# Kernel optimization log

Measured on AMD Instinct MI355X. Metric: run time of the kernel, lower is better.

## Reference

```python
import jax, jax.numpy as jnp
import numpy as np

EMBED = 64
OUT = 64
KERW = 64
DIM = 3

def setup_inputs() -> dict:
    key = jax.random.key(0)
    ks = jax.random.split(key, 6)
    x = jax.random.normal(ks[0], (8, 4096, EMBED), dtype=jnp.float32)
    grid = jax.random.uniform(ks[1], (8, 4096, DIM), dtype=jnp.float32)
    # DenseNet([dim, ker_width_l, output_size*embed_size], GELU): two Linear layers,
    # GELU between, no activation after the last layer.
    W1 = jax.random.normal(ks[2], (DIM, KERW), dtype=jnp.float32) / np.sqrt(DIM)
    b1 = jnp.zeros((KERW,), dtype=jnp.float32)
    W2 = jax.random.normal(ks[3], (KERW, OUT * EMBED), dtype=jnp.float32) / np.sqrt(KERW)
    b2 = jnp.zeros((OUT * EMBED,), dtype=jnp.float32)
    return {"x": x, "grid": grid, "W1": W1, "b1": b1, "W2": W2, "b2": b2}

def reference(x, grid, W1, b1, W2, b2):
    shape = x.shape
    # generator MLP: grid [.., dim] -> per-point weight [.., embed*out]
    h = jax.nn.gelu(grid @ W1 + b1, approximate=False)
    weight = h @ W2 + b2                              # [B, P, embed*out]
    weight = weight.reshape(-1, EMBED, OUT)           # [N, embed, out]
    xf = x.reshape(-1, shape[-1])                     # [N, embed]
    out = jnp.einsum('bi,bio->bo', xf, weight)        # [N, out]
    return out.reshape(*shape[:-1], OUT)
```

## Files before the change

### kernel.cpp

```cpp
#include <hip/hip_runtime.h>
#include <hip/hip_fp16.h>

typedef _Float16 f16x8 __attribute__((ext_vector_type(8)));
typedef float f32x4 __attribute__((ext_vector_type(4)));

#define N_PTS 32768
#define ROWS 64
#define X_STRIDE 72
#define P_STRIDE 68

__global__ __launch_bounds__(256) void prep_kernel(
    const float* __restrict__ W2, const float* __restrict__ b2,
    _Float16* __restrict__ wsB) {
  __shared__ _Float16 w_lds[64][X_STRIDE];
  const int c   = blockIdx.x;
  const int tid = threadIdx.x;
  {
    const float* src = (c < 64) ? (W2 + c * 4096 + tid * 16) : (b2 + tid * 16);
    int kl = tid >> 2, o = (tid & 3) * 16;
    f16x8 v0, v1;
    #pragma unroll
    for (int j = 0; j < 8; ++j) {
      v0[j] = (_Float16)src[j];
      v1[j] = (_Float16)src[8 + j];
    }
    *(f16x8*)(&w_lds[kl][o])     = v0;
    *(f16x8*)(&w_lds[kl][o + 8]) = v1;
  }
  __syncthreads();
  #pragma unroll
  for (int u = 0; u < 2; ++u) {
    int t = tid + u * 256;
    int q = t >> 6, lane = t & 63;
    int klbase = (q >> 2) * 32 + ((lane >> 4) & 3) * 8;
    int o      = (q & 3) * 16 + (lane & 15);
    f16x8 v;
    #pragma unroll
    for (int j = 0; j < 8; ++j) v[j] = w_lds[klbase + j][o];
    *(f16x8*)(wsB + c * 4096 + t * 8) = v;
  }
}

__global__ __launch_bounds__(256) void main_kernel(
    const float* __restrict__ x, const float* __restrict__ gridp,
    const float* __restrict__ W1, const float* __restrict__ b1,
    const _Float16* __restrict__ wsB, float* __restrict__ out) {

  __shared__ _Float16 h_t[4][ROWS][16];
  __shared__ float part[4][ROWS * P_STRIDE];
  _Float16* x_lds = (_Float16*)&part[0][0];

  const int tid  = threadIdx.x;
  const int lane = tid & 63;
  const int wave = tid >> 6;
  const int rowblk = blockIdx.x * ROWS;

  const float* xsrc = x + rowblk * 64 + tid * 16;
  f32x4 xr0 = *(const f32x4*)(xsrc);
  f32x4 xr1 = *(const f32x4*)(xsrc + 4);
  f32x4 xr2 = *(const f32x4*)(xsrc + 8);
  f32x4 xr3 = *(const f32x4*)(xsrc + 12);

  {
    int row = tid >> 2;
    int w4  = tid & 3;
    int r = rowblk + row;
    float g0 = gridp[r * 3 + 0], g1 = gridp[r * 3 + 1], g2 = gridp[r * 3 + 2];
    f16x8 h0, h1;
    #pragma unroll
    for (int q = 0; q < 16; ++q) {
      int k = w4 + 4 * q;
      float v = g0 * W1[k] + g1 * W1[64 + k] + g2 * W1[128 + k] + b1[k];
      float v2 = v * v;
      float u  = v * fmaf(0.044715f, v2, 1.0f);
      float e  = __builtin_amdgcn_exp2f(u * 2.3022084f);
      float rr = e + 1.0f;
      float inv;
      asm("v_rcp_f32 %0, %1" : "=v"(inv) : "v"(rr));
      float h = v * (1.0f - inv);
      if (q < 8) h0[q] = (_Float16)h; else h1[q - 8] = (_Float16)h;
    }
    *(f16x8*)(&h_t[w4][row][0]) = h0;
    *(f16x8*)(&h_t[w4][row][8]) = h1;
  }

  {
    int row = tid >> 2, o = (tid & 3) * 16;
    f16x8 v0, v1;
    #pragma unroll
    for (int j = 0; j < 4; ++j) {
      v0[j]     = (_Float16)xr0[j];
      v0[4 + j] = (_Float16)xr1[j];
      v1[j]     = (_Float16)xr2[j];
      v1[4 + j] = (_Float16)xr3[j];
    }
    *(f16x8*)(&x_lds[row * X_STRIDE + o])     = v0;
    *(f16x8*)(&x_lds[row * X_STRIDE + o + 8]) = v1;
  }
  __syncthreads();

  const int mrow = lane & 15;
  const int kgrp = lane >> 4;
  const _Float16* bp = wsB + lane * 8;

  auto LOADB = [&](f16x8* b, int c) {
    #pragma unroll
    for (int q = 0; q < 8; ++q)
      b[q] = *(const f16x8*)(bp + (c * 8 + q) * 512);
  };

  f16x8 bA[8], bB[8], bC[8];
  LOADB(bA, wave);
  LOADB(bB, wave + 4);
  LOADB(bC, wave + 8);

  f16x8 hreg[4][2];
  #pragma unroll
  for (int m = 0; m < 4; ++m) {
    hreg[m][0] = *(const f16x8*)(&h_t[wave][m * 16 + mrow][0]);
    hreg[m][1] = *(const f16x8*)(&h_t[wave][m * 16 + mrow][8]);
  }

  f16x8 xf[4][2];
  #pragma unroll
  for (int m = 0; m < 4; ++m)
    #pragma unroll
    for (int s = 0; s < 2; ++s)
      xf[m][s] = *(const f16x8*)(&x_lds[(m * 16 + mrow) * X_STRIDE + s * 32 + kgrp * 8]);

  f32x4 acc[4][4];
  #pragma unroll
  for (int m = 0; m < 4; ++m)
    #pragma unroll
    for (int n = 0; n < 4; ++n)
      acc[m][n] = (f32x4){0.f, 0.f, 0.f, 0.f};

  auto COMPUTE = [&](const f16x8* b, int p) {
    __builtin_amdgcn_s_setprio(1);
    #pragma unroll
    for (int m = 0; m < 4; ++m) {
      _Float16 hh = hreg[m][p >> 3][p & 7];
      f16x8 hs = {hh, hh, hh, hh, hh, hh, hh, hh};
      f16x8 a0 = xf[m][0] * hs;
      f16x8 a1 = xf[m][1] * hs;
      #pragma unroll
      for (int n = 0; n < 4; ++n) {
        acc[m][n] = __builtin_amdgcn_mfma_f32_16x16x32_f16(a0, b[n],     acc[m][n], 0, 0, 0);
        acc[m][n] = __builtin_amdgcn_mfma_f32_16x16x32_f16(a1, b[4 + n], acc[m][n], 0, 0, 0);
      }
    }
    __builtin_amdgcn_s_setprio(0);
  };
  auto COMPUTE_BIAS = [&](const f16x8* b) {
    __builtin_amdgcn_s_setprio(1);
    #pragma unroll
    for (int m = 0; m < 4; ++m)
      #pragma unroll
      for (int n = 0; n < 4; ++n) {
        acc[m][n] = __builtin_amdgcn_mfma_f32_16x16x32_f16(xf[m][0], b[n],     acc[m][n], 0, 0, 0);
        acc[m][n] = __builtin_amdgcn_mfma_f32_16x16x32_f16(xf[m][1], b[4 + n], acc[m][n], 0, 0, 0);
      }
    __builtin_amdgcn_s_setprio(0);
  };

  #pragma unroll
  for (int g = 0; g < 5; ++g) {
    COMPUTE(bA, 3 * g);
    if (3 * g + 3 < 16) LOADB(bA, wave + 4 * (3 * g + 3));
    COMPUTE(bB, 3 * g + 1);
    if (3 * g + 4 < 16) LOADB(bB, wave + 4 * (3 * g + 4));
    else if (wave == 0) LOADB(bB, 64);
    COMPUTE(bC, 3 * g + 2);
    if (3 * g + 5 < 16) LOADB(bC, wave + 4 * (3 * g + 5));
  }
  COMPUTE(bA, 15);
  if (wave == 0) COMPUTE_BIAS(bB);

  __syncthreads();

  {
    float* pw = part[wave];
    #pragma unroll
    for (int m = 0; m < 4; ++m)
      #pragma unroll
      for (int n = 0; n < 4; ++n)
        #pragma unroll
        for (int r = 0; r < 4; ++r)
          pw[(m * 16 + kgrp * 4 + r) * P_STRIDE + n * 16 + mrow] = acc[m][n][r];
  }
  __syncthreads();

  {
    int row = tid >> 2;
    int cb  = (tid & 3) * 16;
    const float* p0 = part[0] + row * P_STRIDE + cb;
    float* op = out + (rowblk + row) * 64 + cb;
    #pragma unroll
    for (int j = 0; j < 4; ++j) {
      f32x4 s = *(const f32x4*)(p0 + j * 4);
      #pragma unroll
      for (int w = 1; w < 4; ++w)
        s += *(const f32x4*)(p0 + w * (ROWS * P_STRIDE) + j * 4);
      *(f32x4*)(op + j * 4) = s;
    }
  }
}

extern "C" void kernel_launch(void* const* d_in, const int* in_sizes, int n_in,
                              void* d_out, int out_size, void* d_ws, size_t ws_size,
                              hipStream_t stream) {
  const float* x    = (const float*)d_in[0];
  const float* grid = (const float*)d_in[1];
  const float* W1   = (const float*)d_in[2];
  const float* b1   = (const float*)d_in[3];
  const float* W2   = (const float*)d_in[4];
  const float* b2   = (const float*)d_in[5];
  float* out = (float*)d_out;
  _Float16* wsB = (_Float16*)d_ws;

  hipLaunchKernelGGL(prep_kernel, dim3(65), dim3(256), 0, stream,
                     W2, b2, wsB);
  hipLaunchKernelGGL(main_kernel, dim3(N_PTS / ROWS), dim3(256), 0, stream,
                     x, grid, W1, b1, wsB, out);
}
```

Before: 31.99 us.

## Stagger weight chunk order across blocks, split prep kernel, drop setprio

Odd blocks start the 16-step weight loop at chunk 8 and even blocks at chunk 0, so concurrent blocks read different parts of the shared weight buffer and spread L2/cache traffic. The loop becomes a templated four-buffer rotation that still keeps three loads in flight, with the bias chunk loaded into the freed slot near the end. The prep kernel is split across twice as many blocks, each writing half of a chunk, and the s_setprio hints around the MFMA sections are removed. The two template instantiations double code size, and the extra buffer may raise register pressure.

After: 35.25 us. 10.2% more time.

```diff
diff --git a/kernel.cpp b/kernel.cpp
--- a/kernel.cpp
+++ b/kernel.cpp
@@ -9,11 +9,14 @@
 #define X_STRIDE 72
 #define P_STRIDE 68
 
+template <int V> struct ic { static constexpr int value = V; };
+
 __global__ __launch_bounds__(256) void prep_kernel(
     const float* __restrict__ W2, const float* __restrict__ b2,
     _Float16* __restrict__ wsB) {
   __shared__ _Float16 w_lds[64][X_STRIDE];
-  const int c   = blockIdx.x;
+  const int c   = blockIdx.x >> 1;
+  const int u   = blockIdx.x & 1;
   const int tid = threadIdx.x;
   {
     const float* src = (c < 64) ? (W2 + c * 4096 + tid * 16) : (b2 + tid * 16);
@@ -28,8 +31,7 @@
     *(f16x8*)(&w_lds[kl][o + 8]) = v1;
   }
   __syncthreads();
-  #pragma unroll
-  for (int u = 0; u < 2; ++u) {
+  {
     int t = tid + u * 256;
     int q = t >> 6, lane = t & 63;
     int klbase = (q >> 2) * 32 + ((lane >> 4) & 3) * 8;
@@ -109,10 +111,7 @@
       b[q] = *(const f16x8*)(bp + (c * 8 + q) * 512);
   };
 
-  f16x8 bA[8], bB[8], bC[8];
-  LOADB(bA, wave);
-  LOADB(bB, wave + 4);
-  LOADB(bC, wave + 8);
+  f16x8 buf0[8], buf1[8], buf2[8], buf3[8];
 
   f16x8 hreg[4][2];
   #pragma unroll
@@ -136,7 +135,6 @@
       acc[m][n] = (f32x4){0.f, 0.f, 0.f, 0.f};
 
   auto COMPUTE = [&](const f16x8* b, int p) {
-    __builtin_amdgcn_s_setprio(1);
     #pragma unroll
     for (int m = 0; m < 4; ++m) {
       _Float16 hh = hreg[m][p >> 3][p & 7];
@@ -149,32 +147,37 @@
         acc[m][n] = __builtin_amdgcn_mfma_f32_16x16x32_f16(a1, b[4 + n], acc[m][n], 0, 0, 0);
       }
     }
-    __builtin_amdgcn_s_setprio(0);
   };
-  auto COMPUTE_BIAS = [&](const f16x8* b) {
-    __builtin_amdgcn_s_setprio(1);
-    #pragma unroll
-    for (int m = 0; m < 4; ++m)
-      #pragma unroll
-      for (int n = 0; n < 4; ++n) {
-        acc[m][n] = __builtin_amdgcn_mfma_f32_16x16x32_f16(xf[m][0], b[n],     acc[m][n], 0, 0, 0);
-        acc[m][n] = __builtin_amdgcn_mfma_f32_16x16x32_f16(xf[m][1], b[4 + n], acc[m][n], 0, 0, 0);
+
+  auto runloop = [&](auto p0c) {
+    constexpr int P0 = decltype(p0c)::value;
+    auto P = [](int i) { return ((i + P0) & 15); };
+    f16x8* bufs[4] = {buf0, buf1, buf2, buf3};
+    LOADB(buf0, wave + 4 * P(0));
+    LOADB(buf1, wave + 4 * P(1));
+    LOADB(buf2, wave + 4 * P(2));
+    #pragma unroll
+    for (int i = 0; i < 16; ++i) {
+      f16x8* cur = bufs[i & 3];
+      COMPUTE(cur, P(i));
+      if (i + 3 < 16) {
+        LOADB(bufs[(i + 3) & 3], wave + 4 * P(i + 3));
+      } else if (i == 13 && wave == 0) {
+        LOADB(bufs[0], 64);
       }
-    __builtin_amdgcn_s_setprio(0);
+    }
+    if (wave == 0) {
+      #pragma unroll
+      for (int m = 0; m < 4; ++m)
+        #pragma unroll
+        for (int n = 0; n < 4; ++n) {
+          acc[m][n] = __builtin_amdgcn_mfma_f32_16x16x32_f16(xf[m][0], buf0[n],     acc[m][n], 0, 0, 0);
+          acc[m][n] = __builtin_amdgcn_mfma_f32_16x16x32_f16(xf[m][1], buf0[4 + n], acc[m][n], 0, 0, 0);
+        }
+    }
   };
-
-  #pragma unroll
-  for (int g = 0; g < 5; ++g) {
-    COMPUTE(bA, 3 * g);
-    if (3 * g + 3 < 16) LOADB(bA, wave + 4 * (3 * g + 3));
-    COMPUTE(bB, 3 * g + 1);
-    if (3 * g + 4 < 16) LOADB(bB, wave + 4 * (3 * g + 4));
-    else if (wave == 0) LOADB(bB, 64);
-    COMPUTE(bC, 3 * g + 2);
-    if (3 * g + 5 < 16) LOADB(bC, wave + 4 * (3 * g + 5));
-  }
-  COMPUTE(bA, 15);
-  if (wave == 0) COMPUTE_BIAS(bB);
+  if (blockIdx.x & 1) runloop(ic<8>{});
+  else                runloop(ic<0>{});
 
   __syncthreads();
 
@@ -218,7 +221,7 @@
   float* out = (float*)d_out;
   _Float16* wsB = (_Float16*)d_ws;
 
-  hipLaunchKernelGGL(prep_kernel, dim3(65), dim3(256), 0, stream,
+  hipLaunchKernelGGL(prep_kernel, dim3(130), dim3(256), 0, stream,
                      W2, b2, wsB);
   hipLaunchKernelGGL(main_kernel, dim3(N_PTS / ROWS), dim3(256), 0, stream,
                      x, grid, W1, b1, wsB, out);
```
